# Kernel tuning notes

Hardware: AMD Instinct MI355X
Metric: run time of the kernel (lower is better)

Reference implementation:

```python
import jax, jax.numpy as jnp
import numpy as np

B, L, D, H, W = 32, 1024, 512, 8, 5  # batch, seq, d_model, heads, local_context_length
DK = D // H


def _local_mix(x, W0, b0, w):
    """Sliding-window local-context weighting (faithful to the torch loop version).
    Pads front with w-1 zeros, applies linear (so padded rows become the bias),
    softmax-weights each length-w causal window against the current position,
    and sums the window.  x: [B, L, D] -> [B, L, D]."""
    Bb, Ll, Dd = x.shape
    xp = jnp.pad(x, ((0, 0), (w - 1, 0), (0, 0)))          # [B, L+w-1, D]
    xp = xp @ W0 + b0                                       # linear AFTER pad (padded rows = bias)
    idx = jnp.arange(Ll)[:, None] + jnp.arange(w)[None, :]  # [L, w] window indices into padded seq
    win = xp[:, idx, :]                                     # [B, L, w, D]
    cur = xp[:, w - 1:, :]                                  # [B, L, D] current positions
    scores = jnp.einsum('bld,blwd->blw', cur, win) / jnp.sqrt(jnp.float32(Dd))
    wts = jax.nn.softmax(scores, axis=-1)                   # [B, L, w]
    return jnp.einsum('blw,blwd->bld', wts, win)            # [B, L, D]


def setup_inputs() -> dict:
    rng = jax.random.key(0)
    ks = jax.random.split(rng, 7)
    s = 0.02
    return {
        'query': jax.random.normal(ks[0], (B, L, D), jnp.float32),
        'key':   jax.random.normal(ks[1], (B, L, D), jnp.float32),
        'value': jax.random.normal(ks[2], (B, L, D), jnp.float32),
        'W0':    jax.random.normal(ks[3], (D, D), jnp.float32) * s,
        'b0':    jax.random.normal(ks[4], (D,), jnp.float32) * s,
        'Wout':  jax.random.normal(ks[5], (D, D), jnp.float32) * s,
        'bout':  jax.random.normal(ks[6], (D,), jnp.float32) * s,
    }


def reference(query, key, value, W0, b0, Wout, bout):
    q = _local_mix(query, W0, b0, W).reshape(B, L, H, DK).transpose(0, 2, 1, 3)  # [B,H,L,dk]
    k = _local_mix(key, W0, b0, W).reshape(B, L, H, DK).transpose(0, 2, 1, 3)
    v = (value @ W0 + b0).reshape(B, L, H, DK).transpose(0, 2, 1, 3)
    scores = jnp.einsum('bhqd,bhkd->bhqk', q, k) / jnp.sqrt(jnp.float32(DK))     # [B,H,L,L]
    p = jax.nn.softmax(scores, axis=-1)
    x = jnp.einsum('bhqk,bhkd->bhqd', p, v)
    x = x.transpose(0, 2, 1, 3).reshape(B, L, D)
    return x @ Wout + bout
```

## Files before the change

### kernel.cpp

```cpp
#include <hip/hip_runtime.h>


typedef __attribute__((ext_vector_type(8))) short bf16x8;
typedef __attribute__((ext_vector_type(4))) float f32x4;

#define MFMA16(a, b, c) __builtin_amdgcn_mfma_f32_16x16x32_bf16((a), (b), (c), 0, 0, 0)

static __device__ __forceinline__ float bf2f(unsigned short u) {
  union { unsigned int i; float f; } v; v.i = ((unsigned int)u) << 16; return v.f;
}
static __device__ __forceinline__ unsigned short f2b(float f) {
  union { float fv; unsigned int i; } v; v.fv = f;
  unsigned int u = v.i;
  return (unsigned short)((u + 0x7fffu + ((u >> 16) & 1u)) >> 16);
}
static __device__ __forceinline__ unsigned int cvtpk(float lo, float hi) {
  unsigned int r;
  asm("v_cvt_pk_bf16_f32 %0, %1, %2" : "=v"(r) : "v"(lo), "v"(hi));
  return r;
}
static __device__ __forceinline__ void glds16(const void* g, void* l) {
  __builtin_amdgcn_global_load_lds(
      (const __attribute__((address_space(1))) unsigned int*)g,
      (__attribute__((address_space(3))) unsigned int*)l, 16, 0, 0);
}
static __device__ __forceinline__ void barrier_lgkm() {
  asm volatile("s_waitcnt lgkmcnt(0)" ::: "memory");
  __builtin_amdgcn_s_barrier();
  __builtin_amdgcn_sched_barrier(0);
}

__global__ __launch_bounds__(256) void tcast2_k(const float* __restrict__ s0,
                                                unsigned short* __restrict__ d0,
                                                const float* __restrict__ s1,
                                                unsigned short* __restrict__ d1) {
  int i = blockIdx.x * 256 + threadIdx.x;
  const float* s = s0;
  unsigned short* d = d0;
  if (i >= 262144) { i -= 262144; s = s1; d = d1; }
  int k = i >> 9, n = i & 511;
  d[(size_t)n * 512 + k] = f2b(s[(size_t)k * 512 + n]);
}

template <int AMODE, int OUTMODE>
__device__ __forceinline__ void gemm256(const void* __restrict__ A_,
                                        const unsigned short* __restrict__ BT,
                                        const float* __restrict__ bias,
                                        void* __restrict__ out_, int bm, int bn) {
  __shared__ unsigned short As[2][256 * 64];
  __shared__ unsigned short Bs[2][256 * 64];
  const int tid = threadIdx.x;
  const int w = tid >> 6, l = tid & 63;
  const int lg = l >> 4, lr = l & 15;
  const int wr = w >> 2, wc = w & 3;
  const int rowbase = bm * 256;
  const int colbase = bn * 256;

  const int ar = tid >> 1, kh = tid & 1;
  const int arw = ar & 7;

  f32x4 acc[8][4];
#pragma unroll
  for (int mi = 0; mi < 8; ++mi)
#pragma unroll
    for (int ni = 0; ni < 4; ++ni) acc[mi][ni] = (f32x4){0.f, 0.f, 0.f, 0.f};

  float4 fa[8];
  uint4 ba[4];

  auto loadA = [&](int t) {
    if constexpr (AMODE == 0) {
      const float* p = (const float*)A_ + (size_t)(rowbase + ar) * 512 + t * 64 + kh * 32;
#pragma unroll
      for (int j = 0; j < 8; ++j) fa[j] = ((const float4*)p)[j];
    } else {
      const unsigned short* p = (const unsigned short*)A_ + (size_t)(rowbase + ar) * 512 + t * 64 + kh * 32;
#pragma unroll
      for (int j = 0; j < 4; ++j) ba[j] = ((const uint4*)p)[j];
    }
  };
  auto writeA = [&](int buf) {
    unsigned short* dst = &As[buf][ar * 64];
#pragma unroll
    for (int j = 0; j < 4; ++j) {
      const int g = 4 * kh + j;
      uint4 u;
      if constexpr (AMODE == 0) {
        u.x = cvtpk(fa[2 * j].x, fa[2 * j].y);
        u.y = cvtpk(fa[2 * j].z, fa[2 * j].w);
        u.z = cvtpk(fa[2 * j + 1].x, fa[2 * j + 1].y);
        u.w = cvtpk(fa[2 * j + 1].z, fa[2 * j + 1].w);
      } else {
        u = ba[j];
      }
      *(uint4*)&dst[((g ^ arw) << 3)] = u;
    }
  };
  auto stageB = [&](int t, int buf) {
    const unsigned short* Bt = BT + t * 64;
#pragma unroll
    for (int j = 0; j < 4; ++j) {
      const int jr = j * 64 + w * 8 + (l >> 3);
      const int g = (l & 7) ^ (jr & 7);
      glds16(Bt + (size_t)(colbase + jr) * 512 + g * 8,
             &Bs[buf][(j * 64 + w * 8) * 64]);
    }
  };

  loadA(0);
  stageB(0, 0);
  writeA(0);
  __syncthreads();

  for (int t = 0; t < 8; ++t) {
    const int cur = t & 1;
    if (t < 7) {
      loadA(t + 1);
      stageB(t + 1, cur ^ 1);
    }
#pragma unroll
    for (int ks = 0; ks < 2; ++ks) {
      bf16x8 af[8], bf[4];
#pragma unroll
      for (int ni = 0; ni < 4; ++ni) {
        const int c = wc * 64 + ni * 16 + lr;
        bf[ni] = *(const bf16x8*)&Bs[cur][c * 64 + (((4 * ks + lg) ^ (c & 7)) << 3)];
      }
#pragma unroll
      for (int mi = 0; mi < 8; ++mi) {
        const int r = wr * 128 + mi * 16 + lr;
        af[mi] = *(const bf16x8*)&As[cur][r * 64 + (((4 * ks + lg) ^ (r & 7)) << 3)];
      }
      __builtin_amdgcn_s_setprio(1);
#pragma unroll
      for (int mi = 0; mi < 8; ++mi)
#pragma unroll
        for (int ni = 0; ni < 4; ++ni) acc[mi][ni] = MFMA16(af[mi], bf[ni], acc[mi][ni]);
      __builtin_amdgcn_s_setprio(0);
    }
    if (t < 7) {
      writeA(cur ^ 1);
      __syncthreads();
    }
  }

#pragma unroll
  for (int mi = 0; mi < 8; ++mi)
#pragma unroll
    for (int ni = 0; ni < 4; ++ni) {
      const int grow0 = rowbase + wr * 128 + mi * 16 + 4 * lg;
      const int gcol = colbase + wc * 64 + ni * 16 + lr;
      const float bs = bias[gcol];
#pragma unroll
      for (int r = 0; r < 4; ++r) {
        float v = acc[mi][ni][r] + bs;
        if constexpr (OUTMODE == 0)
          ((unsigned short*)out_)[(size_t)(grow0 + r) * 512 + gcol] = f2b(v);
        else
          ((float*)out_)[(size_t)(grow0 + r) * 512 + gcol] = v;
      }
    }
}

__global__ __launch_bounds__(512) void proj3_k(const float* __restrict__ q,
                                               const float* __restrict__ k,
                                               const float* __restrict__ v,
                                               const unsigned short* __restrict__ W0T,
                                               const float* __restrict__ b0,
                                               unsigned short* __restrict__ Pq,
                                               unsigned short* __restrict__ Pk,
                                               unsigned short* __restrict__ Pv) {
  const int wg = (blockIdx.x & 7) * 96 + (blockIdx.x >> 3);
  const int t = wg >> 8, rem = wg & 255;
  const float* A = t == 0 ? q : t == 1 ? k : v;
  unsigned short* O = t == 0 ? Pq : t == 1 ? Pk : Pv;
  gemm256<0, 0>(A, W0T, b0, O, rem >> 1, rem & 1);
}

__global__ __launch_bounds__(512) void gemmout_k(const unsigned short* __restrict__ A,
                                                 const unsigned short* __restrict__ WoT,
                                                 const float* __restrict__ bout,
                                                 float* __restrict__ out) {
  const int wg = (blockIdx.x & 7) * 32 + (blockIdx.x >> 3);
  gemm256<1, 1>(A, WoT, bout, out, wg >> 1, wg & 1);
}

__global__ __launch_bounds__(256) void localmix2_k(const unsigned short* __restrict__ Pq,
                                                   const unsigned short* __restrict__ Pk,
                                                   const float* __restrict__ b0,
                                                   unsigned short* __restrict__ Qm,
                                                   unsigned short* __restrict__ Km) {
  const int w = threadIdx.x >> 6, lane = threadIdx.x & 63;
  const int pp = blockIdx.x * 4 + w;
  const unsigned short* P;
  unsigned short* out;
  float outscale;
  int p;
  if (pp < 32768) { P = Pq; out = Qm; outscale = 0.18033688011112042f; p = pp; }
  else            { P = Pk; out = Km; outscale = 1.0f; p = pp - 32768; }
  const int l = p & 1023;
  const int d0 = lane * 8;

  float win[5][8];
#pragma unroll
  for (int j = 0; j < 5; ++j) {
    const int src = l - 4 + j;
    if (src >= 0) {
      const uint4 v = *(const uint4*)(P + (size_t)(p - 4 + j) * 512 + d0);
      const unsigned short* u = (const unsigned short*)&v;
#pragma unroll
      for (int i = 0; i < 8; ++i) win[j][i] = bf2f(u[i]);
    } else {
      const float4 f0 = *(const float4*)(b0 + d0);
      const float4 f1 = *(const float4*)(b0 + d0 + 4);
      win[j][0] = f0.x; win[j][1] = f0.y; win[j][2] = f0.z; win[j][3] = f0.w;
      win[j][4] = f1.x; win[j][5] = f1.y; win[j][6] = f1.z; win[j][7] = f1.w;
    }
  }
  float s[5];
#pragma unroll
  for (int j = 0; j < 5; ++j) {
    float t = 0.f;
#pragma unroll
    for (int i = 0; i < 8; ++i) t += win[4][i] * win[j][i];
    s[j] = t;
  }
#pragma unroll
  for (int off = 1; off < 64; off <<= 1)
#pragma unroll
    for (int j = 0; j < 5; ++j) s[j] += __shfl_xor(s[j], off, 64);
  const float sc = 0.04419417382415922f;
  float mx = -1e30f;
#pragma unroll
  for (int j = 0; j < 5; ++j) { s[j] *= sc; mx = fmaxf(mx, s[j]); }
  float e[5], sum = 0.f;
#pragma unroll
  for (int j = 0; j < 5; ++j) { e[j] = __expf(s[j] - mx); sum += e[j]; }
  const float inv = 1.f / sum;
  __attribute__((ext_vector_type(8))) unsigned short o;
#pragma unroll
  for (int i = 0; i < 8; ++i) {
    float a = 0.f;
#pragma unroll
    for (int j = 0; j < 5; ++j) a += e[j] * win[j][i];
    o[i] = f2b(a * inv * outscale);
  }
  *(__attribute__((ext_vector_type(8))) unsigned short*)(out + (size_t)p * 512 + d0) = o;
}

__global__ __launch_bounds__(256) void attn_k(const unsigned short* __restrict__ Q,
                                              const unsigned short* __restrict__ K,
                                              const unsigned short* __restrict__ V,
                                              unsigned short* __restrict__ AO) {
  __shared__ unsigned short Ks[2][64 * 64];
  __shared__ unsigned short Vt[2][64 * 64];
  const int tid = threadIdx.x;
  const int w = tid >> 6, l = tid & 63;
  const int lg = l >> 4, lr = l & 15;
  const int wg = (blockIdx.x & 7) * 256 + (blockIdx.x >> 3);
  const int qt = wg & 7, bh = wg >> 3;
  const int h = bh & 7, b = bh >> 3;
  const size_t base = (size_t)(b * 1024) * 512 + h * 64;
  const unsigned short* Qb = Q + base + (size_t)(qt * 128) * 512;
  const unsigned short* Kb = K + base;
  const unsigned short* Vb = V + base;

  bf16x8 qf[2][2];
#pragma unroll
  for (int rb = 0; rb < 2; ++rb)
#pragma unroll
    for (int ks = 0; ks < 2; ++ks)
      qf[rb][ks] = *(const bf16x8*)(Qb + (size_t)(w * 32 + rb * 16 + lr) * 512 + ks * 32 + lg * 8);

  f32x4 acc[2][4];
#pragma unroll
  for (int rb = 0; rb < 2; ++rb)
#pragma unroll
    for (int nb = 0; nb < 4; ++nb) acc[rb][nb] = (f32x4){0.f, 0.f, 0.f, 0.f};
  float lrun[2] = {0.f, 0.f};

  const int sk_row = tid >> 2, sk_seg = tid & 3;
  const int sv_key = tid & 63, sv_d0 = (tid >> 6) * 16;
  const int vpos = (sv_key & 32) + ((sv_key >> 2) & 3) * 8 + ((sv_key >> 4) & 1) * 4 + (sv_key & 3);
  const int vpg = vpos >> 3, vpw = vpos & 7;
  const int r7 = sk_row & 7;

  uint4 kr0, kr1, vr0, vr1;
  auto loadT = [&](int t) {
    const uint4* ksrc = (const uint4*)(Kb + (size_t)(t * 64 + sk_row) * 512 + sk_seg * 16);
    kr0 = ksrc[0]; kr1 = ksrc[1];
    const uint4* vsrc = (const uint4*)(Vb + (size_t)(t * 64 + sv_key) * 512 + sv_d0);
    vr0 = vsrc[0]; vr1 = vsrc[1];
  };
  auto writeT = [&](int bufi) {
    unsigned short* kd = Ks[bufi];
    unsigned short* vd = Vt[bufi];
    *(uint4*)&kd[sk_row * 64 + (((2 * sk_seg) ^ r7) << 3)] = kr0;
    *(uint4*)&kd[sk_row * 64 + (((2 * sk_seg + 1) ^ r7) << 3)] = kr1;
    const unsigned short* u0 = (const unsigned short*)&vr0;
    const unsigned short* u1 = (const unsigned short*)&vr1;
#pragma unroll
    for (int j = 0; j < 8; ++j) {
      vd[(sv_d0 + j) * 64 + (((vpg ^ j) << 3) | vpw)] = u0[j];
      vd[(sv_d0 + 8 + j) * 64 + (((vpg ^ j) << 3) | vpw)] = u1[j];
    }
  };

  loadT(0);
  writeT(0);
  loadT(1);
  barrier_lgkm();

  const int swz0 = (lg ^ (lr & 7)) << 3, swz1 = ((4 + lg) ^ (lr & 7)) << 3;

  for (int it = 0; it < 16; ++it) {
    const int cur = it & 1;
    f32x4 sf[2][4];
    __builtin_amdgcn_s_setprio(1);
#pragma unroll
    for (int kb = 0; kb < 4; ++kb) {
      const int krow = (kb * 16 + lr) * 64;
      bf16x8 kf0 = *(const bf16x8*)&Ks[cur][krow + swz0];
      bf16x8 kf1 = *(const bf16x8*)&Ks[cur][krow + swz1];
#pragma unroll
      for (int rb = 0; rb < 2; ++rb) {
        f32x4 z = (f32x4){0.f, 0.f, 0.f, 0.f};
        z = MFMA16(kf0, qf[rb][0], z);
        z = MFMA16(kf1, qf[rb][1], z);
        sf[rb][kb] = z;
      }
    }
    __builtin_amdgcn_s_setprio(0);

    if (it < 15) writeT((it + 1) & 1);
    if (it < 14) loadT(it + 2);

#pragma unroll
    for (int rb = 0; rb < 2; ++rb) {
#pragma unroll
      for (int kb = 0; kb < 4; ++kb)
#pragma unroll
        for (int r = 0; r < 4; ++r)
          sf[rb][kb][r] = __builtin_amdgcn_exp2f(sf[rb][kb][r]);
      float s0 = (sf[rb][0][0] + sf[rb][0][1]) + (sf[rb][0][2] + sf[rb][0][3]);
      float s1 = (sf[rb][1][0] + sf[rb][1][1]) + (sf[rb][1][2] + sf[rb][1][3]);
      float s2 = (sf[rb][2][0] + sf[rb][2][1]) + (sf[rb][2][2] + sf[rb][2][3]);
      float s3 = (sf[rb][3][0] + sf[rb][3][1]) + (sf[rb][3][2] + sf[rb][3][3]);
      float t = (s0 + s1) + (s2 + s3);
      t += __shfl_xor(t, 16, 64);
      t += __shfl_xor(t, 32, 64);
      lrun[rb] += t;
    }

    union { uint4 d; bf16x8 v; } pa[2][2];
#pragma unroll
    for (int rb = 0; rb < 2; ++rb)
#pragma unroll
      for (int t2 = 0; t2 < 2; ++t2) {
        pa[rb][t2].d.x = cvtpk(sf[rb][2 * t2][0], sf[rb][2 * t2][1]);
        pa[rb][t2].d.y = cvtpk(sf[rb][2 * t2][2], sf[rb][2 * t2][3]);
        pa[rb][t2].d.z = cvtpk(sf[rb][2 * t2 + 1][0], sf[rb][2 * t2 + 1][1]);
        pa[rb][t2].d.w = cvtpk(sf[rb][2 * t2 + 1][2], sf[rb][2 * t2 + 1][3]);
      }

    __builtin_amdgcn_s_setprio(1);
#pragma unroll
    for (int t2 = 0; t2 < 2; ++t2) {
      bf16x8 vf[4];
#pragma unroll
      for (int nb = 0; nb < 4; ++nb) {
        const int vrow = (nb * 16 + lr) * 64;
        vf[nb] = *(const bf16x8*)&Vt[cur][vrow + (((4 * t2 + lg) ^ (lr & 7)) << 3)];
      }
#pragma unroll
      for (int rb = 0; rb < 2; ++rb)
#pragma unroll
        for (int nb = 0; nb < 4; ++nb) acc[rb][nb] = MFMA16(pa[rb][t2].v, vf[nb], acc[rb][nb]);
    }
    __builtin_amdgcn_s_setprio(0);
    if (it < 15) barrier_lgkm();
  }

#pragma unroll
  for (int rb = 0; rb < 2; ++rb) {
    const float rec = 1.f / lrun[rb];
    float lv[4];
#pragma unroll
    for (int r = 0; r < 4; ++r) lv[r] = __shfl(rec, lg * 4 + r, 64);
#pragma unroll
    for (int nb = 0; nb < 4; ++nb) {
      const int gcol = nb * 16 + lr;
#pragma unroll
      for (int r = 0; r < 4; ++r) {
        const int grow = qt * 128 + w * 32 + rb * 16 + 4 * lg + r;
        AO[base + (size_t)grow * 512 + gcol] = f2b(acc[rb][nb][r] * lv[r]);
      }
    }
  }
}

extern "C" void kernel_launch(void* const* d_in, const int* in_sizes, int n_in,
                              void* d_out, int out_size, void* d_ws, size_t ws_size,
                              hipStream_t stream) {
  const float* query = (const float*)d_in[0];
  const float* key   = (const float*)d_in[1];
  const float* value = (const float*)d_in[2];
  const float* W0    = (const float*)d_in[3];
  const float* b0    = (const float*)d_in[4];
  const float* Wout  = (const float*)d_in[5];
  const float* bout  = (const float*)d_in[6];
  float* out = (float*)d_out;

  char* ws = (char*)d_ws;
  const size_t PSZ = (size_t)32768 * 512 * 2;
  unsigned short* Pq  = (unsigned short*)(ws);
  unsigned short* Pk  = (unsigned short*)(ws + PSZ);
  unsigned short* Pv  = (unsigned short*)(ws + 2 * PSZ);
  unsigned short* Qm  = (unsigned short*)(ws + 3 * PSZ);
  unsigned short* Km  = (unsigned short*)(ws + 4 * PSZ);
  unsigned short* W0T = (unsigned short*)(ws + 5 * PSZ);
  unsigned short* WoT = (unsigned short*)(ws + 5 * PSZ + 524288);

  tcast2_k<<<2048, 256, 0, stream>>>(W0, W0T, Wout, WoT);
  proj3_k<<<768, 512, 0, stream>>>(query, key, value, W0T, b0, Pq, Pk, Pv);
  localmix2_k<<<16384, 256, 0, stream>>>(Pq, Pk, b0, Qm, Km);
  attn_k<<<2048, 256, 0, stream>>>(Qm, Km, Pv, Pq );
  gemmout_k<<<256, 512, 0, stream>>>(Pq, WoT, bout, out);
}
```

Before: 289.2 us.

## Restructure GEMM main loop into finely interleaved 8-phase ping-pong schedule

The 256x256 GEMM main loop is rewritten as an unrolled schedule of eight MFMA phases per pair of k-tiles. B-tile async loads, A register prefetches (two register sets, even and odd) and LDS writes are split into halves and slotted between phases, with explicit barriers and vmcnt waits. The aim is to overlap global loads and LDS writes with MFMA work more evenly and to hide load latency. The launch bounds also request 2 blocks per CU, which puts pressure on registers (extra prefetch buffers, 128 accumulator floats) and risks spills. LDS use is 128 KB per block, which may also limit how many blocks fit per CU.

```diff
diff --git a/kernel.cpp b/kernel.cpp
--- a/kernel.cpp
+++ b/kernel.cpp
@@ -41,6 +41,41 @@
   int k = i >> 9, n = i & 511;
   d[(size_t)n * 512 + k] = f2b(s[(size_t)k * 512 + n]);
 }
+
+#define PREBAR()                          \
+  __builtin_amdgcn_sched_barrier(0);      \
+  __builtin_amdgcn_s_barrier();           \
+  __builtin_amdgcn_sched_barrier(0)
+
+#define ENDP()                            \
+  __builtin_amdgcn_sched_barrier(0);      \
+  __builtin_amdgcn_s_barrier();           \
+  __builtin_amdgcn_sched_barrier(0)
+
+#define ENDPV(N)                                             \
+  asm volatile("s_waitcnt vmcnt(" #N ")" ::: "memory");      \
+  barrier_lgkm()
+
+#define PHASE(bufA, bufB, kk, mh, LOADBF)                                         \
+  {                                                                               \
+    if (LOADBF) {                                                                 \
+      _Pragma("unroll") for (int ni = 0; ni < 4; ++ni) {                          \
+        const int c = wc * 64 + ni * 16 + lr;                                     \
+        bfr[ni] = *(const bf16x8*)&Bs[bufB][c * 64 + (((4 * (kk) + lg) ^ (c & 7)) << 3)]; \
+      }                                                                           \
+    }                                                                             \
+    bf16x8 af[4];                                                                 \
+    _Pragma("unroll") for (int m = 0; m < 4; ++m) {                               \
+      const int r = wr * 128 + ((mh) * 4 + m) * 16 + lr;                          \
+      af[m] = *(const bf16x8*)&As[bufA][r * 64 + (((4 * (kk) + lg) ^ (r & 7)) << 3)]; \
+    }                                                                             \
+    PREBAR();                                                                     \
+    __builtin_amdgcn_s_setprio(1);                                                \
+    _Pragma("unroll") for (int m = 0; m < 4; ++m)                                 \
+      _Pragma("unroll") for (int ni = 0; ni < 4; ++ni)                            \
+        acc[(mh) * 4 + m][ni] = MFMA16(af[m], bfr[ni], acc[(mh) * 4 + m][ni]);    \
+    __builtin_amdgcn_s_setprio(0);                                                \
+  }
 
 template <int AMODE, int OUTMODE>
 __device__ __forceinline__ void gemm256(const void* __restrict__ A_,
@@ -55,9 +90,7 @@
   const int wr = w >> 2, wc = w & 3;
   const int rowbase = bm * 256;
   const int colbase = bn * 256;
-
-  const int ar = tid >> 1, kh = tid & 1;
-  const int arw = ar & 7;
+  const int ar = tid >> 1, kh = tid & 1, arw = ar & 7;
 
   f32x4 acc[8][4];
 #pragma unroll
@@ -65,83 +98,84 @@
 #pragma unroll
     for (int ni = 0; ni < 4; ++ni) acc[mi][ni] = (f32x4){0.f, 0.f, 0.f, 0.f};
 
-  float4 fa[8];
-  uint4 ba[4];
-
-  auto loadA = [&](int t) {
+  float4 pe_f[8], po_f[8];
+  uint4 pe_b[4], po_b[4];
+  bf16x8 bfr[4];
+
+  auto loadA = [&](int t, float4* df, uint4* db) {
     if constexpr (AMODE == 0) {
       const float* p = (const float*)A_ + (size_t)(rowbase + ar) * 512 + t * 64 + kh * 32;
 #pragma unroll
-      for (int j = 0; j < 8; ++j) fa[j] = ((const float4*)p)[j];
+      for (int j = 0; j < 8; ++j) df[j] = ((const float4*)p)[j];
     } else {
       const unsigned short* p = (const unsigned short*)A_ + (size_t)(rowbase + ar) * 512 + t * 64 + kh * 32;
 #pragma unroll
-      for (int j = 0; j < 4; ++j) ba[j] = ((const uint4*)p)[j];
+      for (int j = 0; j < 4; ++j) db[j] = ((const uint4*)p)[j];
     }
   };
-  auto writeA = [&](int buf) {
+  auto writeA = [&](int buf, const float4* df, const uint4* db) {
     unsigned short* dst = &As[buf][ar * 64];
 #pragma unroll
     for (int j = 0; j < 4; ++j) {
       const int g = 4 * kh + j;
       uint4 u;
       if constexpr (AMODE == 0) {
-        u.x = cvtpk(fa[2 * j].x, fa[2 * j].y);
-        u.y = cvtpk(fa[2 * j].z, fa[2 * j].w);
-        u.z = cvtpk(fa[2 * j + 1].x, fa[2 * j + 1].y);
-        u.w = cvtpk(fa[2 * j + 1].z, fa[2 * j + 1].w);
+        u.x = cvtpk(df[2 * j].x, df[2 * j].y);
+        u.y = cvtpk(df[2 * j].z, df[2 * j].w);
+        u.z = cvtpk(df[2 * j + 1].x, df[2 * j + 1].y);
+        u.w = cvtpk(df[2 * j + 1].z, df[2 * j + 1].w);
       } else {
-        u = ba[j];
-      }
-      *(uint4*)&dst[((g ^ arw) << 3)] = u;
+        u = db[j];
+      }
+      *(uint4*)&dst[(g ^ arw) << 3] = u;
     }
   };
-  auto stageB = [&](int t, int buf) {
-    const unsigned short* Bt = BT + t * 64;
-#pragma unroll
-    for (int j = 0; j < 4; ++j) {
+  auto stageBh = [&](int t, int buf, int h) {
+#pragma unroll
+    for (int j = 2 * h; j < 2 * h + 2; ++j) {
       const int jr = j * 64 + w * 8 + (l >> 3);
       const int g = (l & 7) ^ (jr & 7);
-      glds16(Bt + (size_t)(colbase + jr) * 512 + g * 8,
+      glds16(BT + (size_t)(colbase + jr) * 512 + t * 64 + g * 8,
              &Bs[buf][(j * 64 + w * 8) * 64]);
     }
   };
 
-  loadA(0);
-  stageB(0, 0);
-  writeA(0);
-  __syncthreads();
-
-  for (int t = 0; t < 8; ++t) {
-    const int cur = t & 1;
-    if (t < 7) {
-      loadA(t + 1);
-      stageB(t + 1, cur ^ 1);
-    }
-#pragma unroll
-    for (int ks = 0; ks < 2; ++ks) {
-      bf16x8 af[8], bf[4];
-#pragma unroll
-      for (int ni = 0; ni < 4; ++ni) {
-        const int c = wc * 64 + ni * 16 + lr;
-        bf[ni] = *(const bf16x8*)&Bs[cur][c * 64 + (((4 * ks + lg) ^ (c & 7)) << 3)];
-      }
-#pragma unroll
-      for (int mi = 0; mi < 8; ++mi) {
-        const int r = wr * 128 + mi * 16 + lr;
-        af[mi] = *(const bf16x8*)&As[cur][r * 64 + (((4 * ks + lg) ^ (r & 7)) << 3)];
-      }
-      __builtin_amdgcn_s_setprio(1);
-#pragma unroll
-      for (int mi = 0; mi < 8; ++mi)
-#pragma unroll
-        for (int ni = 0; ni < 4; ++ni) acc[mi][ni] = MFMA16(af[mi], bf[ni], acc[mi][ni]);
-      __builtin_amdgcn_s_setprio(0);
-    }
-    if (t < 7) {
-      writeA(cur ^ 1);
-      __syncthreads();
-    }
+  stageBh(0, 0, 0);
+  stageBh(0, 0, 1);
+  loadA(0, pe_f, pe_b);
+  writeA(0, pe_f, pe_b);
+  loadA(1, po_f, po_b);
+  barrier_lgkm();
+
+#pragma unroll
+  for (int i = 0; i < 4; ++i) {
+    const int t = 2 * i;
+    stageBh(t + 1, 1, 0);
+    PHASE(0, 0, 0, 0, true);
+    ENDP();
+    stageBh(t + 1, 1, 1);
+    if (i < 3) loadA(t + 2, pe_f, pe_b);
+    PHASE(0, 0, 0, 1, false);
+    ENDP();
+    writeA(1, po_f, po_b);
+    PHASE(0, 0, 1, 0, true);
+    ENDP();
+    PHASE(0, 0, 1, 1, false);
+    if (i < 3) { ENDPV(8); } else { ENDPV(0); }
+    if (i < 3) stageBh(t + 2, 0, 0);
+    PHASE(1, 1, 0, 0, true);
+    ENDP();
+    if (i < 3) {
+      stageBh(t + 2, 0, 1);
+      writeA(0, pe_f, pe_b);
+    }
+    PHASE(1, 1, 0, 1, false);
+    ENDP();
+    if (i < 3) loadA(t + 3, po_f, po_b);
+    PHASE(1, 1, 1, 0, true);
+    ENDP();
+    PHASE(1, 1, 1, 1, false);
+    ENDPV(8);
   }
 
 #pragma unroll
@@ -162,14 +196,14 @@
     }
 }
 
-__global__ __launch_bounds__(512) void proj3_k(const float* __restrict__ q,
-                                               const float* __restrict__ k,
-                                               const float* __restrict__ v,
-                                               const unsigned short* __restrict__ W0T,
-                                               const float* __restrict__ b0,
-                                               unsigned short* __restrict__ Pq,
-                                               unsigned short* __restrict__ Pk,
-                                               unsigned short* __restrict__ Pv) {
+__global__ __launch_bounds__(512, 2) void proj3_k(const float* __restrict__ q,
+                                                  const float* __restrict__ k,
+                                                  const float* __restrict__ v,
+                                                  const unsigned short* __restrict__ W0T,
+                                                  const float* __restrict__ b0,
+                                                  unsigned short* __restrict__ Pq,
+                                                  unsigned short* __restrict__ Pk,
+                                                  unsigned short* __restrict__ Pv) {
   const int wg = (blockIdx.x & 7) * 96 + (blockIdx.x >> 3);
   const int t = wg >> 8, rem = wg & 255;
   const float* A = t == 0 ? q : t == 1 ? k : v;
@@ -177,10 +211,10 @@
   gemm256<0, 0>(A, W0T, b0, O, rem >> 1, rem & 1);
 }
 
-__global__ __launch_bounds__(512) void gemmout_k(const unsigned short* __restrict__ A,
-                                                 const unsigned short* __restrict__ WoT,
-                                                 const float* __restrict__ bout,
-                                                 float* __restrict__ out) {
+__global__ __launch_bounds__(512, 2) void gemmout_k(const unsigned short* __restrict__ A,
+                                                    const unsigned short* __restrict__ WoT,
+                                                    const float* __restrict__ bout,
+                                                    float* __restrict__ out) {
   const int wg = (blockIdx.x & 7) * 32 + (blockIdx.x >> 3);
   gemm256<1, 1>(A, WoT, bout, out, wg >> 1, wg & 1);
 }
```

Measured after the change: 294.5 us. Within noise of the previous version (+1.8%).
